# Kernel optimization log

Measured on AMD Instinct MI355X. Metric: run time of the kernel, lower is better.

The kernel has to match this reference:

```python
import jax, jax.numpy as jnp
import numpy as np

N = 200_000   # mesh nodes
C = 400_000   # cells (~2N for triangular mesh)
K = 3 * C     # cells_node / cells_index flat length (3 nodes per cell)
E = 600_000   # cell-cell edges (faces)
D = 128       # feature dim
H = 128       # MLP hidden


def setup_inputs() -> dict:
    key = jax.random.key(0)
    ks = jax.random.split(key, 6)
    node_attr = jax.random.normal(ks[0], (N, D), dtype=jnp.float32)
    edge_attr = jax.random.normal(ks[1], (E, D), dtype=jnp.float32)
    W1 = jax.random.normal(ks[2], (3 * D, H), dtype=jnp.float32) * 0.05
    b1 = jnp.zeros((H,), dtype=jnp.float32)
    W2 = jax.random.normal(ks[3], (H, D), dtype=jnp.float32) * 0.05
    b2 = jnp.zeros((D,), dtype=jnp.float32)
    cells_node = jax.random.randint(ks[4], (K,), 0, N, dtype=jnp.int32)
    # each cell owns 3 consecutive node slots (faithful FVM incidence structure)
    cells_index = jnp.repeat(jnp.arange(C, dtype=jnp.int32), 3)
    edge_index = jax.random.randint(ks[5], (2, E), 0, C, dtype=jnp.int32)
    return dict(node_attr=node_attr, edge_attr=edge_attr, W1=W1, b1=b1,
                W2=W2, b2=b2, cells_node=cells_node, cells_index=cells_index,
                edge_index=edge_index)


def reference(node_attr, edge_attr, W1, b1, W2, b2,
              cells_node, cells_index, edge_index):
    # node -> cell scatter-sum (calc_cell_centered_with_node_attr, map=True)
    gathered = node_attr[cells_node]                      # [K, D]
    cell_attr = jax.ops.segment_sum(gathered, cells_index, num_segments=C)  # [C, D]
    senders, receivers = edge_index[0], edge_index[1]
    mask = (senders != receivers)[:, None].astype(node_attr.dtype)  # [E, 1]
    senders_attr = cell_attr[senders]                     # [E, D]
    receivers_attr = cell_attr[receivers] * mask          # zero self-edges
    collected = jnp.concatenate([senders_attr, receivers_attr, edge_attr], axis=1)  # [E, 3D]
    h = jax.nn.relu(collected @ W1 + b1)                  # [E, H]
    edge_attr_new = h @ W2 + b2                           # [E, D]
    return edge_attr_new
```

## Files before the change

### kernel.cpp

```cpp
#include <hip/hip_runtime.h>

typedef short bf16x8 __attribute__((ext_vector_type(8)));
typedef float f32x4 __attribute__((ext_vector_type(4)));

#define MAX_C 400000

__device__ unsigned short g_W1t[384 * 128];
__device__ unsigned short g_W2t[128 * 128];
__device__ unsigned short g_cell[(size_t)MAX_C * 128];

__device__ __forceinline__ unsigned short f2bf(float f) {
    union { unsigned int i; float f; } v; v.f = f;
    unsigned int r = (v.i + 0x7FFFu + ((v.i >> 16) & 1u)) >> 16;
    return (unsigned short)r;
}

__global__ __launch_bounds__(256) void cell_sum_kernel(
        const float* __restrict__ node_attr,
        const int* __restrict__ cells_node, int C)
{
    int t = threadIdx.x;
    int cell = blockIdx.x * 16 + (t >> 4);
    int sub = t & 15;
    if (cell >= C || cell >= MAX_C) return;
    float acc[8] = {0.f,0.f,0.f,0.f,0.f,0.f,0.f,0.f};
    #pragma unroll
    for (int j = 0; j < 3; ++j) {
        int idx = cells_node[cell * 3 + j];
        const float* p = node_attr + (long)idx * 128 + sub * 8;
        float4 v0 = *(const float4*)(p);
        float4 v1 = *(const float4*)(p + 4);
        acc[0] += v0.x; acc[1] += v0.y; acc[2] += v0.z; acc[3] += v0.w;
        acc[4] += v1.x; acc[5] += v1.y; acc[6] += v1.z; acc[7] += v1.w;
    }
    unsigned short o[8];
    #pragma unroll
    for (int q = 0; q < 8; ++q) o[q] = f2bf(acc[q]);
    *(uint4*)(g_cell + (long)cell * 128 + sub * 8) = *(const uint4*)o;
}

__global__ __launch_bounds__(256) void wprep_kernel(
        const float* __restrict__ W1,
        const float* __restrict__ W2)
{
    int i = blockIdx.x * 256 + threadIdx.x;
    if (i < 384 * 128) {
        int n = i / 384, k = i % 384;
        g_W1t[i] = f2bf(W1[k * 128 + n]);
    } else {
        int j = i - 384 * 128;
        int n = j / 128, k = j % 128;
        g_W2t[j] = f2bf(W2[k * 128 + n]);
    }
}

__global__ __launch_bounds__(256) void edge_mlp_kernel(
        const float* __restrict__ edge_attr,
        const float* __restrict__ b1,
        const float* __restrict__ b2,
        const int* __restrict__ senders,
        const int* __restrict__ receivers,
        float* __restrict__ out, int E)
{
    __shared__ __align__(16) unsigned char smem[1024 + 10240 + 34816];
    int* sIdx = (int*)smem;
    int* rIdx = (int*)(smem + 512);
    unsigned short* Wts = (unsigned short*)(smem + 1024);
    unsigned short* As  = (unsigned short*)(smem + 1024 + 10240);
    unsigned short* Hs  = (unsigned short*)(smem + 1024 + 10240);

    int t = threadIdx.x;
    int e0 = blockIdx.x * 128;

    if (t < 128) sIdx[t] = senders[min(e0 + t, E - 1)];
    else         rIdx[t - 128] = receivers[min(e0 + t - 128, E - 1)];
    __syncthreads();

    int wv = t >> 6, l = t & 63;
    int lrow = l & 15, quad = l >> 4;

    f32x4 acc[2][8];
    #pragma unroll
    for (int m = 0; m < 2; ++m)
        #pragma unroll
        for (int n = 0; n < 8; ++n) acc[m][n] = (f32x4)(0.f);

    for (int kc = 0; kc < 12; ++kc) {
        int kin = (kc & 3) * 32;
        #pragma unroll
        for (int i = 0; i < 2; ++i) {
            int tau = t + i * 256;
            int row = tau >> 2;
            int koff = (tau & 3) * 8;
            uint4 v;
            if (kc < 4) {
                v = *(const uint4*)(g_cell + (long)sIdx[row] * 128 + kin + koff);
            } else if (kc < 8) {
                if (sIdx[row] == rIdx[row]) v = make_uint4(0u, 0u, 0u, 0u);
                else v = *(const uint4*)(g_cell + (long)rIdx[row] * 128 + kin + koff);
            } else {
                int e = min(e0 + row, E - 1);
                const float* p = edge_attr + (long)e * 128 + kin + koff;
                float4 f0 = *(const float4*)(p);
                float4 f1 = *(const float4*)(p + 4);
                unsigned short tmp[8];
                tmp[0] = f2bf(f0.x); tmp[1] = f2bf(f0.y);
                tmp[2] = f2bf(f0.z); tmp[3] = f2bf(f0.w);
                tmp[4] = f2bf(f1.x); tmp[5] = f2bf(f1.y);
                tmp[6] = f2bf(f1.z); tmp[7] = f2bf(f1.w);
                v = *(const uint4*)tmp;
            }
            *(uint4*)(As + row * 40 + koff) = v;
            uint4 w = *(const uint4*)(g_W1t + (long)row * 384 + kc * 32 + koff);
            *(uint4*)(Wts + row * 40 + koff) = w;
        }
        __syncthreads();
        bf16x8 a0 = *(const bf16x8*)(As + (wv * 32 + lrow) * 40 + quad * 8);
        bf16x8 a1 = *(const bf16x8*)(As + (wv * 32 + 16 + lrow) * 40 + quad * 8);
        #pragma unroll
        for (int nt = 0; nt < 8; ++nt) {
            bf16x8 b = *(const bf16x8*)(Wts + (nt * 16 + lrow) * 40 + quad * 8);
            acc[0][nt] = __builtin_amdgcn_mfma_f32_16x16x32_bf16(a0, b, acc[0][nt], 0, 0, 0);
            acc[1][nt] = __builtin_amdgcn_mfma_f32_16x16x32_bf16(a1, b, acc[1][nt], 0, 0, 0);
        }
        __syncthreads();
    }

    #pragma unroll
    for (int m = 0; m < 2; ++m) {
        int rbase = wv * 32 + m * 16 + quad * 4;
        #pragma unroll
        for (int nt = 0; nt < 8; ++nt) {
            int n = nt * 16 + lrow;
            float bias = b1[n];
            #pragma unroll
            for (int r = 0; r < 4; ++r) {
                float v = acc[m][nt][r] + bias;
                v = v > 0.f ? v : 0.f;
                Hs[(rbase + r) * 136 + n] = f2bf(v);
            }
        }
    }
    __syncthreads();

    f32x4 acc2[2][8];
    #pragma unroll
    for (int m = 0; m < 2; ++m)
        #pragma unroll
        for (int n = 0; n < 8; ++n) acc2[m][n] = (f32x4)(0.f);

    for (int kc = 0; kc < 4; ++kc) {
        #pragma unroll
        for (int i = 0; i < 2; ++i) {
            int tau = t + i * 256;
            int row = tau >> 2;
            int koff = (tau & 3) * 8;
            uint4 w = *(const uint4*)(g_W2t + (long)row * 128 + kc * 32 + koff);
            *(uint4*)(Wts + row * 40 + koff) = w;
        }
        __syncthreads();
        bf16x8 a0 = *(const bf16x8*)(Hs + (wv * 32 + lrow) * 136 + kc * 32 + quad * 8);
        bf16x8 a1 = *(const bf16x8*)(Hs + (wv * 32 + 16 + lrow) * 136 + kc * 32 + quad * 8);
        #pragma unroll
        for (int nt = 0; nt < 8; ++nt) {
            bf16x8 b = *(const bf16x8*)(Wts + (nt * 16 + lrow) * 40 + quad * 8);
            acc2[0][nt] = __builtin_amdgcn_mfma_f32_16x16x32_bf16(a0, b, acc2[0][nt], 0, 0, 0);
            acc2[1][nt] = __builtin_amdgcn_mfma_f32_16x16x32_bf16(a1, b, acc2[1][nt], 0, 0, 0);
        }
        __syncthreads();
    }

    #pragma unroll
    for (int m = 0; m < 2; ++m) {
        int rbase = wv * 32 + m * 16 + quad * 4;
        #pragma unroll
        for (int nt = 0; nt < 8; ++nt) {
            int n = nt * 16 + lrow;
            float bias = b2[n];
            #pragma unroll
            for (int r = 0; r < 4; ++r) {
                int e = e0 + rbase + r;
                if (e < E) out[(long)e * 128 + n] = acc2[m][nt][r] + bias;
            }
        }
    }
}

extern "C" void kernel_launch(void* const* d_in, const int* in_sizes, int n_in,
                              void* d_out, int out_size, void* d_ws, size_t ws_size,
                              hipStream_t stream)
{
    const float* node_attr = (const float*)d_in[0];
    const float* edge_attr = (const float*)d_in[1];
    const float* W1 = (const float*)d_in[2];
    const float* b1 = (const float*)d_in[3];
    const float* W2 = (const float*)d_in[4];
    const float* b2 = (const float*)d_in[5];
    const int* cells_node  = (const int*)d_in[6];
    const int* edge_index  = (const int*)d_in[8];
    float* out = (float*)d_out;

    int E = in_sizes[1] / 128;
    int C = in_sizes[6] / 3;

    const int* senders = edge_index;
    const int* receivers = edge_index + E;

    hipLaunchKernelGGL(cell_sum_kernel, dim3((C + 15) / 16), dim3(256), 0, stream,
                       node_attr, cells_node, C);
    hipLaunchKernelGGL(wprep_kernel, dim3((384 * 128 + 128 * 128) / 256), dim3(256), 0, stream,
                       W1, W2);
    hipLaunchKernelGGL(edge_mlp_kernel, dim3((E + 127) / 128), dim3(256), 0, stream,
                       edge_attr, b1, b2, senders, receivers, out, E);
}
```

Before: 834.9 us.

## Load MFMA operands straight from global into registers with double buffering

The edge MLP kernel no longer stages gathered cell rows and weights through shared memory with barriers per K-chunk. Each lane loads its bf16x8 fragments directly from global into a double-buffered register set, with weights as the A operand and gathered rows as B. Self-edges point to an extra zero row instead of taking a branch. A prep kernel now also converts edge_attr to bf16 ahead of time and handles two cells per thread group. The second GEMM keeps W2 fragments in registers, and output is written with float4 stores. In exchange there is extra global traffic to write and re-read the bf16 edge copy, and register pressure rises from the held fragments.

```diff
diff --git a/kernel.cpp b/kernel.cpp
--- a/kernel.cpp
+++ b/kernel.cpp
@@ -4,39 +4,83 @@
 typedef float f32x4 __attribute__((ext_vector_type(4)));
 
 #define MAX_C 400000
-
-__device__ unsigned short g_W1t[384 * 128];
-__device__ unsigned short g_W2t[128 * 128];
-__device__ unsigned short g_cell[(size_t)MAX_C * 128];
+#define MAX_E 600000
+
+__device__ __align__(16) unsigned short g_W1t[128 * 384];
+__device__ __align__(16) unsigned short g_W2t[128 * 128];
+__device__ __align__(16) unsigned short g_cell[((size_t)MAX_C + 1) * 128];
+__device__ __align__(16) unsigned short g_edge[(size_t)MAX_E * 128];
 
 __device__ __forceinline__ unsigned short f2bf(float f) {
     union { unsigned int i; float f; } v; v.f = f;
-    unsigned int r = (v.i + 0x7FFFu + ((v.i >> 16) & 1u)) >> 16;
-    return (unsigned short)r;
-}
-
-__global__ __launch_bounds__(256) void cell_sum_kernel(
+    return (unsigned short)((v.i + 0x7FFFu + ((v.i >> 16) & 1u)) >> 16);
+}
+
+__global__ __launch_bounds__(256) void prep_kernel(
         const float* __restrict__ node_attr,
-        const int* __restrict__ cells_node, int C)
+        const float* __restrict__ edge_attr,
+        const int* __restrict__ cells_node,
+        int C, int E, int cellBlocks)
 {
     int t = threadIdx.x;
-    int cell = blockIdx.x * 16 + (t >> 4);
-    int sub = t & 15;
-    if (cell >= C || cell >= MAX_C) return;
-    float acc[8] = {0.f,0.f,0.f,0.f,0.f,0.f,0.f,0.f};
-    #pragma unroll
-    for (int j = 0; j < 3; ++j) {
-        int idx = cells_node[cell * 3 + j];
-        const float* p = node_attr + (long)idx * 128 + sub * 8;
+    if ((int)blockIdx.x < cellBlocks) {
+        int grp = blockIdx.x * 16 + (t >> 4);
+        int sub = t & 15;
+        int c0 = grp * 2, c1 = c0 + 1;
+        if (c0 >= C || c0 >= MAX_C) return;
+        int ja[3], jb[3];
+        ja[0] = cells_node[c0 * 3 + 0];
+        ja[1] = cells_node[c0 * 3 + 1];
+        ja[2] = cells_node[c0 * 3 + 2];
+        bool d1 = (c1 < C) && (c1 < MAX_C);
+        jb[0] = d1 ? cells_node[c1 * 3 + 0] : ja[0];
+        jb[1] = d1 ? cells_node[c1 * 3 + 1] : ja[1];
+        jb[2] = d1 ? cells_node[c1 * 3 + 2] : ja[2];
+
+        float a0[8] = {0.f,0.f,0.f,0.f,0.f,0.f,0.f,0.f};
+        float a1[8] = {0.f,0.f,0.f,0.f,0.f,0.f,0.f,0.f};
+        #pragma unroll
+        for (int j = 0; j < 3; ++j) {
+            const float* p = node_attr + (size_t)ja[j] * 128 + sub * 8;
+            float4 v0 = *(const float4*)(p);
+            float4 v1 = *(const float4*)(p + 4);
+            a0[0] += v0.x; a0[1] += v0.y; a0[2] += v0.z; a0[3] += v0.w;
+            a0[4] += v1.x; a0[5] += v1.y; a0[6] += v1.z; a0[7] += v1.w;
+        }
+        #pragma unroll
+        for (int j = 0; j < 3; ++j) {
+            const float* p = node_attr + (size_t)jb[j] * 128 + sub * 8;
+            float4 v0 = *(const float4*)(p);
+            float4 v1 = *(const float4*)(p + 4);
+            a1[0] += v0.x; a1[1] += v0.y; a1[2] += v0.z; a1[3] += v0.w;
+            a1[4] += v1.x; a1[5] += v1.y; a1[6] += v1.z; a1[7] += v1.w;
+        }
+        uint4 o0, o1;
+        o0.x = (unsigned)f2bf(a0[0]) | ((unsigned)f2bf(a0[1]) << 16);
+        o0.y = (unsigned)f2bf(a0[2]) | ((unsigned)f2bf(a0[3]) << 16);
+        o0.z = (unsigned)f2bf(a0[4]) | ((unsigned)f2bf(a0[5]) << 16);
+        o0.w = (unsigned)f2bf(a0[6]) | ((unsigned)f2bf(a0[7]) << 16);
+        *(uint4*)(g_cell + (size_t)c0 * 128 + sub * 8) = o0;
+        if (d1) {
+            o1.x = (unsigned)f2bf(a1[0]) | ((unsigned)f2bf(a1[1]) << 16);
+            o1.y = (unsigned)f2bf(a1[2]) | ((unsigned)f2bf(a1[3]) << 16);
+            o1.z = (unsigned)f2bf(a1[4]) | ((unsigned)f2bf(a1[5]) << 16);
+            o1.w = (unsigned)f2bf(a1[6]) | ((unsigned)f2bf(a1[7]) << 16);
+            *(uint4*)(g_cell + (size_t)c1 * 128 + sub * 8) = o1;
+        }
+    } else {
+        long i = (long)((int)blockIdx.x - cellBlocks) * 256 + t;
+        if (i >= (long)E * 16) return;
+        const float* p = edge_attr + i * 8;
         float4 v0 = *(const float4*)(p);
         float4 v1 = *(const float4*)(p + 4);
-        acc[0] += v0.x; acc[1] += v0.y; acc[2] += v0.z; acc[3] += v0.w;
-        acc[4] += v1.x; acc[5] += v1.y; acc[6] += v1.z; acc[7] += v1.w;
-    }
-    unsigned short o[8];
-    #pragma unroll
-    for (int q = 0; q < 8; ++q) o[q] = f2bf(acc[q]);
-    *(uint4*)(g_cell + (long)cell * 128 + sub * 8) = *(const uint4*)o;
+        uint4 o;
+        o.x = (unsigned)f2bf(v0.x) | ((unsigned)f2bf(v0.y) << 16);
+        o.y = (unsigned)f2bf(v0.z) | ((unsigned)f2bf(v0.w) << 16);
+        o.z = (unsigned)f2bf(v1.x) | ((unsigned)f2bf(v1.y) << 16);
+        o.w = (unsigned)f2bf(v1.z) | ((unsigned)f2bf(v1.w) << 16);
+        *(uint4*)(g_edge + i * 8) = o;
+    }
 }
 
 __global__ __launch_bounds__(256) void wprep_kernel(
@@ -55,132 +99,137 @@
 }
 
 __global__ __launch_bounds__(256) void edge_mlp_kernel(
-        const float* __restrict__ edge_attr,
         const float* __restrict__ b1,
         const float* __restrict__ b2,
         const int* __restrict__ senders,
         const int* __restrict__ receivers,
         float* __restrict__ out, int E)
 {
-    __shared__ __align__(16) unsigned char smem[1024 + 10240 + 34816];
-    int* sIdx = (int*)smem;
-    int* rIdx = (int*)(smem + 512);
-    unsigned short* Wts = (unsigned short*)(smem + 1024);
-    unsigned short* As  = (unsigned short*)(smem + 1024 + 10240);
-    unsigned short* Hs  = (unsigned short*)(smem + 1024 + 10240);
-
-    int t = threadIdx.x;
-    int e0 = blockIdx.x * 128;
-
-    if (t < 128) sIdx[t] = senders[min(e0 + t, E - 1)];
-    else         rIdx[t - 128] = receivers[min(e0 + t - 128, E - 1)];
+    __shared__ __align__(16) unsigned short Hs[128][136];
+
+    const int t  = threadIdx.x;
+    const int e0 = blockIdx.x * 128;
+    const int wv = t >> 6;
+    const int l  = t & 63;
+    const int lr = l & 15;
+    const int q  = l >> 4;
+
+    unsigned os[8], orr[8], oe[8];
+    #pragma unroll
+    for (int nt = 0; nt < 8; ++nt) {
+        int e = e0 + nt * 16 + lr;
+        if (e > E - 1) e = E - 1;
+        int s = senders[e];
+        int r = receivers[e];
+        os[nt]  = (unsigned)s * 256u;
+        orr[nt] = (s == r) ? (unsigned)MAX_C * 256u : (unsigned)r * 256u;
+        oe[nt]  = (unsigned)e * 256u;
+    }
+
+    const unsigned qb  = (unsigned)(q * 16);
+    const unsigned ow0 = (unsigned)((wv * 32 + lr) * 768) + qb;
+    const unsigned ow1 = ow0 + 16u * 768u;
+
+    const char* cellb = (const char*)g_cell;
+    const char* edgeb = (const char*)g_edge;
+    const char* w1b   = (const char*)g_W1t;
+    const char* w2b   = (const char*)g_W2t;
+
+    f32x4 acc[2][8];
+    #pragma unroll
+    for (int m = 0; m < 2; ++m)
+        #pragma unroll
+        for (int nt = 0; nt < 8; ++nt) acc[m][nt] = (f32x4)(0.f);
+
+    bf16x8 aF[2][2], bF[2][8];
+
+    auto l1load = [&](int kc, int p) {
+        if (kc < 4) {
+            #pragma unroll
+            for (int nt = 0; nt < 8; ++nt)
+                bF[p][nt] = *(const bf16x8*)(cellb + (size_t)(os[nt] + qb + kc * 64));
+        } else if (kc < 8) {
+            #pragma unroll
+            for (int nt = 0; nt < 8; ++nt)
+                bF[p][nt] = *(const bf16x8*)(cellb + (size_t)(orr[nt] + qb + (kc - 4) * 64));
+        } else {
+            #pragma unroll
+            for (int nt = 0; nt < 8; ++nt)
+                bF[p][nt] = *(const bf16x8*)(edgeb + (size_t)(oe[nt] + qb + (kc - 8) * 64));
+        }
+        aF[p][0] = *(const bf16x8*)(w1b + (size_t)(ow0 + kc * 64));
+        aF[p][1] = *(const bf16x8*)(w1b + (size_t)(ow1 + kc * 64));
+    };
+
+    l1load(0, 0);
+    #pragma unroll
+    for (int kc = 0; kc < 12; ++kc) {
+        const int cur = kc & 1;
+        if (kc + 1 < 12) l1load(kc + 1, cur ^ 1);
+        #pragma unroll
+        for (int nt = 0; nt < 8; ++nt) {
+            acc[0][nt] = __builtin_amdgcn_mfma_f32_16x16x32_bf16(aF[cur][0], bF[cur][nt], acc[0][nt], 0, 0, 0);
+            acc[1][nt] = __builtin_amdgcn_mfma_f32_16x16x32_bf16(aF[cur][1], bF[cur][nt], acc[1][nt], 0, 0, 0);
+        }
+    }
+
+    #pragma unroll
+    for (int m = 0; m < 2; ++m) {
+        const int hc = wv * 32 + m * 16 + q * 4;
+        const float4 bv = *(const float4*)(b1 + hc);
+        #pragma unroll
+        for (int nt = 0; nt < 8; ++nt) {
+            float v0 = acc[m][nt][0] + bv.x; v0 = v0 > 0.f ? v0 : 0.f;
+            float v1 = acc[m][nt][1] + bv.y; v1 = v1 > 0.f ? v1 : 0.f;
+            float v2 = acc[m][nt][2] + bv.z; v2 = v2 > 0.f ? v2 : 0.f;
+            float v3 = acc[m][nt][3] + bv.w; v3 = v3 > 0.f ? v3 : 0.f;
+            uint2 w;
+            w.x = (unsigned)f2bf(v0) | ((unsigned)f2bf(v1) << 16);
+            w.y = (unsigned)f2bf(v2) | ((unsigned)f2bf(v3) << 16);
+            *(uint2*)&Hs[nt * 16 + lr][hc] = w;
+        }
+    }
+
+    const unsigned ow20 = (unsigned)((wv * 32 + lr) * 256) + qb;
+    const unsigned ow21 = ow20 + 16u * 256u;
+    bf16x8 w2f[2][4];
+    #pragma unroll
+    for (int kc = 0; kc < 4; ++kc) {
+        w2f[0][kc] = *(const bf16x8*)(w2b + (size_t)(ow20 + kc * 64));
+        w2f[1][kc] = *(const bf16x8*)(w2b + (size_t)(ow21 + kc * 64));
+    }
     __syncthreads();
 
-    int wv = t >> 6, l = t & 63;
-    int lrow = l & 15, quad = l >> 4;
-
-    f32x4 acc[2][8];
+    f32x4 acc2[2][8];
     #pragma unroll
     for (int m = 0; m < 2; ++m)
         #pragma unroll
-        for (int n = 0; n < 8; ++n) acc[m][n] = (f32x4)(0.f);
-
-    for (int kc = 0; kc < 12; ++kc) {
-        int kin = (kc & 3) * 32;
-        #pragma unroll
-        for (int i = 0; i < 2; ++i) {
-            int tau = t + i * 256;
-            int row = tau >> 2;
-            int koff = (tau & 3) * 8;
-            uint4 v;
-            if (kc < 4) {
-                v = *(const uint4*)(g_cell + (long)sIdx[row] * 128 + kin + koff);
-            } else if (kc < 8) {
-                if (sIdx[row] == rIdx[row]) v = make_uint4(0u, 0u, 0u, 0u);
-                else v = *(const uint4*)(g_cell + (long)rIdx[row] * 128 + kin + koff);
-            } else {
-                int e = min(e0 + row, E - 1);
-                const float* p = edge_attr + (long)e * 128 + kin + koff;
-                float4 f0 = *(const float4*)(p);
-                float4 f1 = *(const float4*)(p + 4);
-                unsigned short tmp[8];
-                tmp[0] = f2bf(f0.x); tmp[1] = f2bf(f0.y);
-                tmp[2] = f2bf(f0.z); tmp[3] = f2bf(f0.w);
-                tmp[4] = f2bf(f1.x); tmp[5] = f2bf(f1.y);
-                tmp[6] = f2bf(f1.z); tmp[7] = f2bf(f1.w);
-                v = *(const uint4*)tmp;
-            }
-            *(uint4*)(As + row * 40 + koff) = v;
-            uint4 w = *(const uint4*)(g_W1t + (long)row * 384 + kc * 32 + koff);
-            *(uint4*)(Wts + row * 40 + koff) = w;
-        }
-        __syncthreads();
-        bf16x8 a0 = *(const bf16x8*)(As + (wv * 32 + lrow) * 40 + quad * 8);
-        bf16x8 a1 = *(const bf16x8*)(As + (wv * 32 + 16 + lrow) * 40 + quad * 8);
-        #pragma unroll
-        for (int nt = 0; nt < 8; ++nt) {
-            bf16x8 b = *(const bf16x8*)(Wts + (nt * 16 + lrow) * 40 + quad * 8);
-            acc[0][nt] = __builtin_amdgcn_mfma_f32_16x16x32_bf16(a0, b, acc[0][nt], 0, 0, 0);
-            acc[1][nt] = __builtin_amdgcn_mfma_f32_16x16x32_bf16(a1, b, acc[1][nt], 0, 0, 0);
-        }
-        __syncthreads();
+        for (int nt = 0; nt < 8; ++nt) acc2[m][nt] = (f32x4)(0.f);
+
+    #pragma unroll
+    for (int kc = 0; kc < 4; ++kc) {
+        #pragma unroll
+        for (int nt = 0; nt < 8; ++nt) {
+            bf16x8 b = *(const bf16x8*)&Hs[nt * 16 + lr][kc * 32 + q * 8];
+            acc2[0][nt] = __builtin_amdgcn_mfma_f32_16x16x32_bf16(w2f[0][kc], b, acc2[0][nt], 0, 0, 0);
+            acc2[1][nt] = __builtin_amdgcn_mfma_f32_16x16x32_bf16(w2f[1][kc], b, acc2[1][nt], 0, 0, 0);
+        }
     }
 
     #pragma unroll
     for (int m = 0; m < 2; ++m) {
-        int rbase = wv * 32 + m * 16 + quad * 4;
-        #pragma unroll
-        for (int nt = 0; nt < 8; ++nt) {
-            int n = nt * 16 + lrow;
-            float bias = b1[n];
-            #pragma unroll
-            for (int r = 0; r < 4; ++r) {
-                float v = acc[m][nt][r] + bias;
-                v = v > 0.f ? v : 0.f;
-                Hs[(rbase + r) * 136 + n] = f2bf(v);
-            }
-        }
-    }
-    __syncthreads();
-
-    f32x4 acc2[2][8];
-    #pragma unroll
-    for (int m = 0; m < 2; ++m)
-        #pragma unroll
-        for (int n = 0; n < 8; ++n) acc2[m][n] = (f32x4)(0.f);
-
-    for (int kc = 0; kc < 4; ++kc) {
-        #pragma unroll
-        for (int i = 0; i < 2; ++i) {
-            int tau = t + i * 256;
-            int row = tau >> 2;
-            int koff = (tau & 3) * 8;
-            uint4 w = *(const uint4*)(g_W2t + (long)row * 128 + kc * 32 + koff);
-            *(uint4*)(Wts + row * 40 + koff) = w;
-        }
-        __syncthreads();
-        bf16x8 a0 = *(const bf16x8*)(Hs + (wv * 32 + lrow) * 136 + kc * 32 + quad * 8);
-        bf16x8 a1 = *(const bf16x8*)(Hs + (wv * 32 + 16 + lrow) * 136 + kc * 32 + quad * 8);
-        #pragma unroll
-        for (int nt = 0; nt < 8; ++nt) {
-            bf16x8 b = *(const bf16x8*)(Wts + (nt * 16 + lrow) * 40 + quad * 8);
-            acc2[0][nt] = __builtin_amdgcn_mfma_f32_16x16x32_bf16(a0, b, acc2[0][nt], 0, 0, 0);
-            acc2[1][nt] = __builtin_amdgcn_mfma_f32_16x16x32_bf16(a1, b, acc2[1][nt], 0, 0, 0);
-        }
-        __syncthreads();
-    }
-
-    #pragma unroll
-    for (int m = 0; m < 2; ++m) {
-        int rbase = wv * 32 + m * 16 + quad * 4;
-        #pragma unroll
-        for (int nt = 0; nt < 8; ++nt) {
-            int n = nt * 16 + lrow;
-            float bias = b2[n];
-            #pragma unroll
-            for (int r = 0; r < 4; ++r) {
-                int e = e0 + rbase + r;
-                if (e < E) out[(long)e * 128 + n] = acc2[m][nt][r] + bias;
+        const int oc = wv * 32 + m * 16 + q * 4;
+        const float4 bv = *(const float4*)(b2 + oc);
+        #pragma unroll
+        for (int nt = 0; nt < 8; ++nt) {
+            int e = e0 + nt * 16 + lr;
+            if (e < E) {
+                float4 v;
+                v.x = acc2[m][nt][0] + bv.x;
+                v.y = acc2[m][nt][1] + bv.y;
+                v.z = acc2[m][nt][2] + bv.z;
+                v.w = acc2[m][nt][3] + bv.w;
+                *(float4*)(out + (size_t)e * 128 + oc) = v;
             }
         }
     }
@@ -206,10 +255,13 @@
     const int* senders = edge_index;
     const int* receivers = edge_index + E;
 
-    hipLaunchKernelGGL(cell_sum_kernel, dim3((C + 15) / 16), dim3(256), 0, stream,
-                       node_attr, cells_node, C);
+    int cellBlocks = (C + 31) / 32;
+    int edgeBlocks = (int)(((long)E * 16 + 255) / 256);
+
+    hipLaunchKernelGGL(prep_kernel, dim3(cellBlocks + edgeBlocks), dim3(256), 0, stream,
+                       node_attr, edge_attr, cells_node, C, E, cellBlocks);
     hipLaunchKernelGGL(wprep_kernel, dim3((384 * 128 + 128 * 128) / 256), dim3(256), 0, stream,
                        W1, W2);
     hipLaunchKernelGGL(edge_mlp_kernel, dim3((E + 127) / 128), dim3(256), 0, stream,
-                       edge_attr, b1, b2, senders, receivers, out, E);
-}
+                       b1, b2, senders, receivers, out, E);
+}
```

Result: slower. 1.035 ms (+23.9%).
